# Optimization experiments

Hardware: AMD Instinct MI355X
Metric: run time of the kernel (lower is better)

The kernel has to match this reference:

```python
import jax, jax.numpy as jnp
import numpy as np

B, S, D = 2, 2048, 2048
NH, HD = 32, 64          # query heads, head_dim
NKV, NREP = 8, 4         # kv heads, num_key_value_groups
ROPE_THETA = 10000.0


def _rope_cos_sin(seq_len, head_dim, dtype=jnp.float32):
    inv_freq = 1.0 / (ROPE_THETA ** (jnp.arange(0, head_dim, 2, dtype=jnp.float32) / head_dim))
    pos = jnp.arange(seq_len, dtype=jnp.float32)
    freqs = jnp.outer(pos, inv_freq)               # [S, HD/2]
    emb = jnp.concatenate([freqs, freqs], axis=-1)  # [S, HD]
    return jnp.cos(emb).astype(dtype), jnp.sin(emb).astype(dtype)


def _rotate_half(x):
    x1, x2 = jnp.split(x, 2, axis=-1)
    return jnp.concatenate([-x2, x1], axis=-1)


def setup_inputs() -> dict:
    key = jax.random.key(0)
    k1, k2, k3, k4, k5 = jax.random.split(key, 5)
    scale = 0.02
    hidden_states = jax.random.normal(k1, (B, S, D), dtype=jnp.float32)
    Wq = jax.random.normal(k2, (NH * HD, D), dtype=jnp.float32) * scale
    Wk = jax.random.normal(k3, (NKV * HD, D), dtype=jnp.float32) * scale
    Wv = jax.random.normal(k4, (NKV * HD, D), dtype=jnp.float32) * scale
    Wo = jax.random.normal(k5, (D, NH * HD), dtype=jnp.float32) * scale
    # additive causal mask [B, 1, S, S]: 0 on/below diagonal, large negative above
    causal = jnp.triu(jnp.full((S, S), -1e9, dtype=jnp.float32), k=1)
    attention_mask = jnp.broadcast_to(causal[None, None], (B, 1, S, S))
    return {"hidden_states": hidden_states, "Wq": Wq, "Wk": Wk, "Wv": Wv,
            "Wo": Wo, "attention_mask": attention_mask}


def reference(hidden_states, Wq, Wk, Wv, Wo, attention_mask):
    bsz, q_len, _ = hidden_states.shape
    # projections (torch Linear: x @ W^T)
    q = (hidden_states @ Wq.T).reshape(bsz, q_len, NH, HD).transpose(0, 2, 1, 3)   # [B,NH,S,HD]
    k = (hidden_states @ Wk.T).reshape(bsz, q_len, NKV, HD).transpose(0, 2, 1, 3)  # [B,NKV,S,HD]
    v = (hidden_states @ Wv.T).reshape(bsz, q_len, NKV, HD).transpose(0, 2, 1, 3)
    # RoPE
    cos, sin = _rope_cos_sin(q_len, HD, hidden_states.dtype)  # [S,HD]
    cos = cos[None, None]  # [1,1,S,HD] (unsqueeze_dim=1 over broadcast batch)
    sin = sin[None, None]
    q = q * cos + _rotate_half(q) * sin
    k = k * cos + _rotate_half(k) * sin
    # repeat_kv (GQA): [B,NKV,S,HD] -> [B,NH,S,HD]
    k = jnp.repeat(k, NREP, axis=1)
    v = jnp.repeat(v, NREP, axis=1)
    # eager attention with materialized scores (faithful to the source)
    scores = jnp.einsum('bhqd,bhkd->bhqk', q, k) / jnp.sqrt(jnp.float32(HD))
    scores = scores + attention_mask[:, :, :, :q_len]
    probs = jax.nn.softmax(scores.astype(jnp.float32), axis=-1).astype(q.dtype)
    out = jnp.einsum('bhqk,bhkd->bhqd', probs, v)          # [B,NH,S,HD]
    out = out.transpose(0, 2, 1, 3).reshape(bsz, q_len, NH * HD)
    return out @ Wo.T
```

## Files before the change

kernel.cpp:

```cpp
#include <hip/hip_runtime.h>


#define S_LEN 2048
#define D_MODEL 2048
#define NHEAD 32
#define HEAD_DIM 64
#define NKVH 8
#define M_ROWS 4096
#define KVW (NKVH * HEAD_DIM)

typedef __attribute__((ext_vector_type(4))) float f32x4;
typedef __attribute__((ext_vector_type(8))) short bf16x8;

#define MFMA16(a, b, c) __builtin_amdgcn_mfma_f32_16x16x32_bf16((a), (b), (c), 0, 0, 0)

#define GLOAD_LDS16(g, l)                                                     \
    __builtin_amdgcn_global_load_lds(                                         \
        (const __attribute__((address_space(1))) void*)(g),                   \
        (__attribute__((address_space(3))) void*)(l), 16, 0, 0)

static __device__ __forceinline__ unsigned short f2bf(float f) {
    union { __bf16 b; unsigned short u; } v;
    v.b = (__bf16)f;
    return v.u;
}

static __device__ __forceinline__ void xcd_swz(int& bx, int& by) {
    const int gx = gridDim.x;
    const int nwg = gx * gridDim.y;
    int lin = blockIdx.y * gx + blockIdx.x;
    lin = (lin & 7) * (nwg >> 3) + (lin >> 3);
    bx = lin % gx;
    by = lin / gx;
}

static __device__ bool detect_f32_block(const unsigned short* __restrict__ h) {
    __shared__ int dcnt;
    if (threadIdx.x == 0) dcnt = 0;
    __syncthreads();
    const unsigned short v = h[2 * (threadIdx.x & 255)];
    const int e = (v >> 7) & 0xFF;
    if (threadIdx.x < 256 && e >= 0x8D) atomicAdd(&dcnt, 1);
    __syncthreads();
    return dcnt >= 8;
}

static __device__ __forceinline__ bf16x8 load_frag(bool f32p, const void* p, size_t off) {
    if (f32p) {
        const float* fp = (const float*)p + off;
        f32x4 x = *reinterpret_cast<const f32x4*>(fp);
        f32x4 y = *reinterpret_cast<const f32x4*>(fp + 4);
        bf16x8 r;
        r[0] = (short)f2bf(x[0]); r[1] = (short)f2bf(x[1]);
        r[2] = (short)f2bf(x[2]); r[3] = (short)f2bf(x[3]);
        r[4] = (short)f2bf(y[0]); r[5] = (short)f2bf(y[1]);
        r[6] = (short)f2bf(y[2]); r[7] = (short)f2bf(y[3]);
        return r;
    }
    return *reinterpret_cast<const bf16x8*>((const unsigned short*)p + off);
}

__global__ __launch_bounds__(256) void cvt_all(const void* __restrict__ h,
                                               const void* __restrict__ wq,
                                               const void* __restrict__ wk,
                                               const void* __restrict__ wv,
                                               const void* __restrict__ wo,
                                               unsigned short* __restrict__ hbuf,
                                               unsigned short* __restrict__ wqb,
                                               unsigned short* __restrict__ wkvb,
                                               unsigned short* __restrict__ wob,
                                               float2* __restrict__ ropetab) {
    const bool f32p = detect_f32_block((const unsigned short*)h);
    const int e0 = 1048576;
    const int e1 = e0 + 524288;
    const int e2 = e1 + 131072;
    const int e3 = e2 + 131072;
    const int e4 = e3 + 524288;
    const int e5 = e4 + 8192;
    int i = blockIdx.x * 256 + threadIdx.x;
    const int stride = gridDim.x * 256;
    for (; i < e5; i += stride) {
        if (i >= e4) {
            const int base = (i - e4) * 8;
#pragma unroll
            for (int j = 0; j < 8; ++j) {
                const int idx = base + j;
                const int s = idx >> 5, dd = idx & 31;
                const float inv = exp2f(-(float)dd * 0.4152410118609203f);
                const float th = (float)s * inv;
                float sn, cs;
                sincosf(th, &sn, &cs);
                ropetab[idx] = make_float2(cs, sn);
            }
            continue;
        }
        const void* s;
        unsigned short* d;
        size_t off;
        if (i < e0)      { s = h;  d = hbuf; off = (size_t)i; }
        else if (i < e1) { s = wq; d = wqb;  off = (size_t)(i - e0); }
        else if (i < e2) { s = wk; d = wkvb; off = (size_t)(i - e1); }
        else if (i < e3) { s = wv; d = wkvb + (size_t)512 * 2048; off = (size_t)(i - e2); }
        else             { s = wo; d = wob;  off = (size_t)(i - e3); }
        bf16x8 v = load_frag(f32p, s, off * 8);
        *reinterpret_cast<bf16x8*>(d + off * 8) = v;
    }
}

static __device__ __forceinline__ void rope4_tab(const float2* __restrict__ tab,
                                                 const float (&vals)[4], float (&outv)[4],
                                                 int m, int l16) {
    const int s = m & (S_LEN - 1);
#pragma unroll
    for (int nt = 0; nt < 4; ++nt) {
        const int d = nt * 16 + l16;
        const float2 cs = tab[s * 32 + (d & 31)];
        const float part = vals[nt ^ 2];
        const float rot = (nt < 2) ? -part : part;
        outv[nt] = vals[nt] * cs.x + rot * cs.y;
    }
}

static __device__ __forceinline__ void rope4(const float (&vals)[4], float (&outv)[4],
                                             int m, int l16) {
    const float sf = (float)(m & (S_LEN - 1));
#pragma unroll
    for (int nt = 0; nt < 4; ++nt) {
        const int d = nt * 16 + l16;
        const float inv = exp2f(-(float)(d & 31) * 0.4152410118609203f);
        const float th = sf * inv;
        float sn, cs;
        sincosf(th, &sn, &cs);
        const float part = vals[nt ^ 2];
        const float rot = (nt < 2) ? -part : part;
        outv[nt] = vals[nt] * cs + rot * sn;
    }
}

#define GEMM_STAGE(BB, KK)                                                    \
    {                                                                         \
        _Pragma("unroll")                                                     \
        for (int i_ = 0; i_ < 2; ++i_) {                                      \
            const int c_ = wave * 2 + i_;                                     \
            GLOAD_LDS16(ag[i_] + (KK), &lds_a[BB][c_ * 512]);                 \
            GLOAD_LDS16(wg[i_] + (KK), &lds_b[BB][c_ * 512]);                 \
        }                                                                     \
    }

#define GEMM_MAINLOOP()                                                       \
    GEMM_STAGE(0, 0);                                                         \
    __syncthreads();                                                          \
    {                                                                         \
        int cur = 0;                                                          \
        for (int k0 = 0; k0 < D_MODEL; k0 += 32) {                            \
            if (k0 + 32 < D_MODEL) GEMM_STAGE(cur ^ 1, k0 + 32);              \
            bf16x8 af[4], bfm[4];                                             \
            _Pragma("unroll")                                                 \
            for (int t = 0; t < 4; ++t) {                                     \
                af[t]  = *reinterpret_cast<const bf16x8*>(                    \
                    &lds_a[cur][(wm * 64 + t * 16 + l16) * 32 + quad * 8]);   \
                bfm[t] = *reinterpret_cast<const bf16x8*>(                    \
                    &lds_b[cur][(wn * 64 + t * 16 + l16) * 32 + quad * 8]);   \
            }                                                                 \
            _Pragma("unroll")                                                 \
            for (int mt = 0; mt < 4; ++mt)                                    \
                _Pragma("unroll")                                             \
                for (int nt = 0; nt < 4; ++nt)                                \
                    acc[mt][nt] = MFMA16(af[mt], bfm[nt], acc[mt][nt]);       \
            __syncthreads();                                                  \
            cur ^= 1;                                                         \
        }                                                                     \
    }

__global__ __launch_bounds__(256) void gemm_qkv_lds(const unsigned short* __restrict__ A,
                                                    const unsigned short* __restrict__ W,
                                                    unsigned short* __restrict__ Qo,
                                                    unsigned short* __restrict__ KVo,
                                                    const float2* __restrict__ ropetab) {
    __shared__ unsigned short lds_a[2][128 * 32];
    __shared__ unsigned short lds_b[2][128 * 32];

    const int wave = threadIdx.x >> 6;
    const int lane = threadIdx.x & 63;
    const int l16  = lane & 15;
    const int quad = lane >> 4;
    const int wm   = wave >> 1;
    const int wn   = wave & 1;

    int bx, by;
    xcd_swz(bx, by);
    const int m0 = bx * 128;
    const int n0 = by * 128;

    const int srow = lane >> 2;
    const int scol = (lane & 3) * 8;
    const unsigned short* ag[2];
    const unsigned short* wg[2];
#pragma unroll
    for (int i = 0; i < 2; ++i) {
        const int c = wave * 2 + i;
        ag[i] = A + (size_t)(m0 + c * 16 + srow) * D_MODEL + scol;
        wg[i] = W + (size_t)(n0 + c * 16 + srow) * D_MODEL + scol;
    }

    f32x4 acc[4][4];
#pragma unroll
    for (int i = 0; i < 4; ++i)
#pragma unroll
        for (int j = 0; j < 4; ++j) acc[i][j] = (f32x4){0.f, 0.f, 0.f, 0.f};

    GEMM_MAINLOOP();

    const int ncol0 = n0 + wn * 64;
    const bool do_rope = (ncol0 < 2048 + KVW);
    unsigned short* dst;
    int cstride, c0;
    if (ncol0 < 2048) { dst = Qo;  cstride = 2048; c0 = ncol0; }
    else              { dst = KVo; cstride = 1024; c0 = ncol0 - 2048; }

#pragma unroll
    for (int mt = 0; mt < 4; ++mt) {
#pragma unroll
        for (int r = 0; r < 4; ++r) {
            const int m = m0 + wm * 64 + mt * 16 + quad * 4 + r;
            float vals[4];
#pragma unroll
            for (int nt = 0; nt < 4; ++nt) vals[nt] = acc[mt][nt][r];
            float outv[4];
            if (do_rope) {
                rope4_tab(ropetab, vals, outv, m, l16);
            } else {
#pragma unroll
                for (int nt = 0; nt < 4; ++nt) outv[nt] = vals[nt];
            }
            unsigned short* cp = dst + (size_t)m * cstride + c0;
#pragma unroll
            for (int nt = 0; nt < 4; ++nt) cp[nt * 16 + l16] = f2bf(outv[nt]);
        }
    }
}

__global__ __launch_bounds__(256) void gemm_bt_lds(const unsigned short* __restrict__ A,
                                                   const unsigned short* __restrict__ W,
                                                   void* __restrict__ Cp, int N,
                                                   const unsigned short* __restrict__ hdet,
                                                   int rope, int finalout) {
    __shared__ unsigned short lds_a[2][128 * 32];
    __shared__ unsigned short lds_b[2][128 * 32];

    bool of32 = false;
    if (finalout) of32 = detect_f32_block(hdet);

    const int wave = threadIdx.x >> 6;
    const int lane = threadIdx.x & 63;
    const int l16  = lane & 15;
    const int quad = lane >> 4;
    const int wm   = wave >> 1;
    const int wn   = wave & 1;

    int bx, by;
    xcd_swz(bx, by);
    const int m0 = bx * 128;
    const int n0 = by * 128;

    const int srow = lane >> 2;
    const int scol = (lane & 3) * 8;
    const unsigned short* ag[2];
    const unsigned short* wg[2];
#pragma unroll
    for (int i = 0; i < 2; ++i) {
        const int c = wave * 2 + i;
        ag[i] = A + (size_t)(m0 + c * 16 + srow) * D_MODEL + scol;
        wg[i] = W + (size_t)(n0 + c * 16 + srow) * D_MODEL + scol;
    }

    f32x4 acc[4][4];
#pragma unroll
    for (int i = 0; i < 4; ++i)
#pragma unroll
        for (int j = 0; j < 4; ++j) acc[i][j] = (f32x4){0.f, 0.f, 0.f, 0.f};

    GEMM_MAINLOOP();

    const bool do_rope = (rope != 0);
    const int ncol0 = n0 + wn * 64;

#pragma unroll
    for (int mt = 0; mt < 4; ++mt) {
#pragma unroll
        for (int r = 0; r < 4; ++r) {
            const int m = m0 + wm * 64 + mt * 16 + quad * 4 + r;
            float vals[4];
#pragma unroll
            for (int nt = 0; nt < 4; ++nt) vals[nt] = acc[mt][nt][r];
            float outv[4];
            if (do_rope) {
                rope4(vals, outv, m, l16);
            } else {
#pragma unroll
                for (int nt = 0; nt < 4; ++nt) outv[nt] = vals[nt];
            }
            const size_t crow = (size_t)m * N + ncol0;
            if (of32) {
                float* cp = (float*)Cp + crow;
#pragma unroll
                for (int nt = 0; nt < 4; ++nt) cp[nt * 16 + l16] = outv[nt];
            } else {
                unsigned short* cp = (unsigned short*)Cp + crow;
#pragma unroll
                for (int nt = 0; nt < 4; ++nt) cp[nt * 16 + l16] = f2bf(outv[nt]);
            }
        }
    }
}

__global__ __launch_bounds__(256) void transpose_v(const unsigned short* __restrict__ Vsrc,
                                                   unsigned short* __restrict__ Vt) {
    __shared__ unsigned short t[64][72];
    const int bid = blockIdx.x;
    const int ct = bid & 7;
    const int st = (bid >> 3) & 31;
    const int b  = bid >> 8;
    const unsigned short* src = Vsrc + ((size_t)b * S_LEN + st * 64) * 1024 + ct * 64;
    unsigned short* dst = Vt + ((size_t)b * KVW + ct * 64) * S_LEN + st * 64;
    const int r0 = threadIdx.x >> 3;
    const int c0 = (threadIdx.x & 7) * 8;
#pragma unroll
    for (int h = 0; h < 2; ++h) {
        bf16x8 v = *reinterpret_cast<const bf16x8*>(src + (size_t)(r0 + h * 32) * 1024 + c0);
        *reinterpret_cast<bf16x8*>(&t[r0 + h * 32][c0]) = v;
    }
    __syncthreads();
#pragma unroll
    for (int h = 0; h < 2; ++h) {
        const int cr = r0 + h * 32;
        bf16x8 v;
#pragma unroll
        for (int j = 0; j < 8; ++j) v[j] = (short)t[c0 + j][cr];
        *reinterpret_cast<bf16x8*>(dst + (size_t)cr * S_LEN + c0) = v;
    }
}

struct AttnCtx {
    const unsigned short* qbase;
    const unsigned short* kbase;
    const unsigned short* vtbase;
    unsigned short* obase;
    int kvs;
    int l16, quad;
    unsigned short (*lpw)[72];
};

#define SM_SCALE 0.125f
#define SM_THR_E 5.545177444479562f

static __device__ __forceinline__ void attn_qtile(const AttnCtx& cx, int q0w) {
    const int l16 = cx.l16, quad = cx.quad;
    const int kvs = cx.kvs;

    bf16x8 ones;
#pragma unroll
    for (int j = 0; j < 8; ++j) ones[j] = (short)0x3F80;

    bf16x8 aq[2][2];
#pragma unroll
    for (int m = 0; m < 2; ++m)
#pragma unroll
        for (int kh = 0; kh < 2; ++kh)
            aq[m][kh] = *reinterpret_cast<const bf16x8*>(
                cx.qbase + (size_t)(q0w + m * 16 + l16) * D_MODEL + kh * 32 + quad * 8);

    f32x4 o[2][4];
    f32x4 c_l[2];
#pragma unroll
    for (int m = 0; m < 2; ++m) {
#pragma unroll
        for (int i = 0; i < 4; ++i) o[m][i] = (f32x4){0.f, 0.f, 0.f, 0.f};
        c_l[m] = (f32x4){0.f, 0.f, 0.f, 0.f};
    }
    float m2[2][4];
#pragma unroll
    for (int m = 0; m < 2; ++m)
#pragma unroll
        for (int r = 0; r < 4; ++r) m2[m][r] = 0.f;

    const int kv_hi = q0w + 32;

    for (int k0 = 0; k0 < kv_hi; k0 += 64) {
        bf16x8 kf[8];
#pragma unroll
        for (int t = 0; t < 4; ++t) {
            const unsigned short* krow = cx.kbase + (size_t)(k0 + t * 16 + l16) * kvs;
            kf[2 * t]     = *reinterpret_cast<const bf16x8*>(krow + quad * 8);
            kf[2 * t + 1] = *reinterpret_cast<const bf16x8*>(krow + 32 + quad * 8);
        }

        f32x4 sc[2][4];
        __builtin_amdgcn_s_setprio(1);
#pragma unroll
        for (int t = 0; t < 4; ++t) {
#pragma unroll
            for (int m = 0; m < 2; ++m) {
                f32x4 c = (f32x4){0.f, 0.f, 0.f, 0.f};
                c = MFMA16(aq[m][0], kf[2 * t], c);
                c = MFMA16(aq[m][1], kf[2 * t + 1], c);
                sc[m][t] = c;
            }
        }
        __builtin_amdgcn_s_setprio(0);

        bf16x8 vf[8];
#pragma unroll
        for (int nt = 0; nt < 4; ++nt) {
            const unsigned short* vrow =
                cx.vtbase + (size_t)(nt * 16 + l16) * S_LEN + k0 + quad * 8;
            vf[2 * nt]     = *reinterpret_cast<const bf16x8*>(vrow);
            vf[2 * nt + 1] = *reinterpret_cast<const bf16x8*>(vrow + 32);
        }

        const bool full = (k0 + 63 <= q0w);
        float pm[2][4];
        float dif = -3.0e38f;
#pragma unroll
        for (int m = 0; m < 2; ++m) {
#pragma unroll
            for (int r = 0; r < 4; ++r) {
                const int qi = q0w + m * 16 + quad * 4 + r;
                float s[4];
#pragma unroll
                for (int t = 0; t < 4; ++t) {
                    s[t] = sc[m][t][r] * SM_SCALE;
                    if (!full && (k0 + t * 16 + l16 > qi)) s[t] = -1.0e30f;
                    sc[m][t][r] = s[t];
                }
                const float p = fmaxf(fmaxf(s[0], s[1]), fmaxf(s[2], s[3]));
                pm[m][r] = p;
                dif = fmaxf(dif, p - m2[m][r]);
            }
        }
        if (__any(dif > SM_THR_E)) {
#pragma unroll
            for (int m = 0; m < 2; ++m) {
#pragma unroll
                for (int r = 0; r < 4; ++r) {
                    float mt = pm[m][r];
#pragma unroll
                    for (int off = 1; off < 16; off <<= 1)
                        mt = fmaxf(mt, __shfl_xor(mt, off, 64));
                    const float mn = fmaxf(m2[m][r], mt);
                    const float al = __expf(m2[m][r] - mn);
                    m2[m][r] = mn;
#pragma unroll
                    for (int nt = 0; nt < 4; ++nt) o[m][nt][r] *= al;
                    c_l[m][r] *= al;
                }
            }
        }
#pragma unroll
        for (int m = 0; m < 2; ++m) {
#pragma unroll
            for (int r = 0; r < 4; ++r) {
                const float mb = m2[m][r];
#pragma unroll
                for (int t = 0; t < 4; ++t) {
                    const float pv = __expf(sc[m][t][r] - mb);
                    cx.lpw[m * 16 + quad * 4 + r][t * 16 + l16] = f2bf(pv);
                }
            }
        }
        asm volatile("" ::: "memory");
        bf16x8 ap[2][2];
#pragma unroll
        for (int m = 0; m < 2; ++m)
#pragma unroll
            for (int kh = 0; kh < 2; ++kh)
                ap[m][kh] = *reinterpret_cast<const bf16x8*>(
                    &cx.lpw[m * 16 + l16][kh * 32 + quad * 8]);
        __builtin_amdgcn_s_setprio(1);
#pragma unroll
        for (int nt = 0; nt < 4; ++nt)
#pragma unroll
            for (int m = 0; m < 2; ++m) {
                o[m][nt] = MFMA16(ap[m][0], vf[2 * nt], o[m][nt]);
                o[m][nt] = MFMA16(ap[m][1], vf[2 * nt + 1], o[m][nt]);
            }
#pragma unroll
        for (int m = 0; m < 2; ++m) {
            c_l[m] = MFMA16(ap[m][0], ones, c_l[m]);
            c_l[m] = MFMA16(ap[m][1], ones, c_l[m]);
        }
        __builtin_amdgcn_s_setprio(0);
    }

#pragma unroll
    for (int m = 0; m < 2; ++m)
#pragma unroll
        for (int r = 0; r < 4; ++r) {
            const float inv_l = 1.0f / c_l[m][r];
            unsigned short* orow = cx.obase + (size_t)(q0w + m * 16 + quad * 4 + r) * D_MODEL;
#pragma unroll
            for (int nt = 0; nt < 4; ++nt)
                orow[nt * 16 + l16] = f2bf(o[m][nt][r] * inv_l);
        }
}

__global__ __launch_bounds__(256) void attn_kernel8(const unsigned short* __restrict__ Q,
                                                    const unsigned short* __restrict__ Kb,
                                                    const unsigned short* __restrict__ Vt,
                                                    unsigned short* __restrict__ O, int kvs) {
    __shared__ unsigned short lp[4][32][72];

    const int wave = threadIdx.x >> 6;
    const int lane = threadIdx.x & 63;

    const int bid  = blockIdx.x;
    const int qt   = 15 - (bid >> 6);
    const int bh   = bid & 63;
    const int h    = bh & (NHEAD - 1);
    const int b    = bh >> 5;
    const int kvh  = h >> 2;

    AttnCtx cx;
    cx.qbase  = Q + (size_t)b * S_LEN * D_MODEL + h * HEAD_DIM;
    cx.kbase  = Kb + (size_t)b * S_LEN * kvs + kvh * HEAD_DIM;
    cx.vtbase = Vt + ((size_t)b * KVW + kvh * HEAD_DIM) * S_LEN;
    cx.obase  = O + (size_t)b * S_LEN * D_MODEL + h * HEAD_DIM;
    cx.kvs    = kvs;
    cx.l16    = lane & 15;
    cx.quad   = lane >> 4;
    cx.lpw    = lp[wave];

    attn_qtile(cx, qt * 128 + wave * 32);
}

__global__ __launch_bounds__(256) void gemm_bt(const void* __restrict__ Ap,
                                               const void* __restrict__ Wp,
                                               void* __restrict__ Cp, int N,
                                               const unsigned short* __restrict__ hdet,
                                               int a_input, int rope, int finalout) {
    const bool isf32 = detect_f32_block(hdet);
    const bool af32 = isf32 && (a_input != 0);
    const bool wf32 = isf32;
    const bool of32 = isf32 && (finalout != 0);

    const int wave = threadIdx.x >> 6;
    const int lane = threadIdx.x & 63;
    const int l16  = lane & 15;
    const int quad = lane >> 4;
    const int m0 = blockIdx.x * 64 + wave * 16;
    const int n0 = blockIdx.y * 64;

    f32x4 acc[4];
#pragma unroll
    for (int i = 0; i < 4; ++i) acc[i] = (f32x4){0.f, 0.f, 0.f, 0.f};

    const size_t aoff = (size_t)(m0 + l16) * D_MODEL + quad * 8;
    size_t woff[4];
#pragma unroll
    for (int nt = 0; nt < 4; ++nt)
        woff[nt] = (size_t)(n0 + nt * 16 + l16) * D_MODEL + quad * 8;

    for (int k0 = 0; k0 < D_MODEL; k0 += 32) {
        bf16x8 a = load_frag(af32, Ap, aoff + k0);
#pragma unroll
        for (int nt = 0; nt < 4; ++nt) {
            bf16x8 b = load_frag(wf32, Wp, woff[nt] + k0);
            acc[nt] = MFMA16(a, b, acc[nt]);
        }
    }

#pragma unroll
    for (int r = 0; r < 4; ++r) {
        const int m = m0 + quad * 4 + r;
        float vals[4];
#pragma unroll
        for (int nt = 0; nt < 4; ++nt) vals[nt] = acc[nt][r];
        float outv[4];
        if (rope) {
            rope4(vals, outv, m, l16);
        } else {
#pragma unroll
            for (int nt = 0; nt < 4; ++nt) outv[nt] = vals[nt];
        }
        const size_t crow = (size_t)m * N + n0;
        if (of32) {
            float* cp = (float*)Cp + crow;
#pragma unroll
            for (int nt = 0; nt < 4; ++nt) cp[nt * 16 + l16] = outv[nt];
        } else {
            unsigned short* cp = (unsigned short*)Cp + crow;
#pragma unroll
            for (int nt = 0; nt < 4; ++nt) cp[nt * 16 + l16] = f2bf(outv[nt]);
        }
    }
}

__global__ __launch_bounds__(256) void attn_kernel(const unsigned short* __restrict__ Q,
                                                   const unsigned short* __restrict__ Kb,
                                                   const unsigned short* __restrict__ Vb,
                                                   unsigned short* __restrict__ O, int kvs) {
    __shared__ unsigned short lp[4][16][32];

    const int wave = threadIdx.x >> 6;
    const int lane = threadIdx.x & 63;
    const int l16  = lane & 15;
    const int quad = lane >> 4;

    const int bid = blockIdx.x;
    const int qb  = bid & 31;
    const int h   = (bid >> 5) & 31;
    const int b   = bid >> 10;
    const int kvh = h >> 2;
    const int q0  = qb * 64 + wave * 16;

    const unsigned short* qbase = Q + (size_t)b * S_LEN * D_MODEL + h * HEAD_DIM;
    const unsigned short* kbase = Kb + (size_t)b * S_LEN * kvs + kvh * HEAD_DIM;
    const unsigned short* vbase = Vb + (size_t)b * S_LEN * kvs + kvh * HEAD_DIM;

    bf16x8 aq0 = *reinterpret_cast<const bf16x8*>(qbase + (size_t)(q0 + l16) * D_MODEL + quad * 8);
    bf16x8 aq1 = *reinterpret_cast<const bf16x8*>(qbase + (size_t)(q0 + l16) * D_MODEL + 32 + quad * 8);

    f32x4 o[4];
#pragma unroll
    for (int i = 0; i < 4; ++i) o[i] = (f32x4){0.f, 0.f, 0.f, 0.f};
    float mrow[4], lrow[4];
#pragma unroll
    for (int r = 0; r < 4; ++r) { mrow[r] = -3.0e38f; lrow[r] = 0.f; }

    const int kv_hi = qb * 64 + 64;
    for (int k0 = 0; k0 < kv_hi; k0 += 32) {
        f32x4 sc[2];
#pragma unroll
        for (int t = 0; t < 2; ++t) {
            const unsigned short* krow = kbase + (size_t)(k0 + t * 16 + l16) * kvs;
            bf16x8 b0 = *reinterpret_cast<const bf16x8*>(krow + quad * 8);
            bf16x8 b1 = *reinterpret_cast<const bf16x8*>(krow + 32 + quad * 8);
            f32x4 c = (f32x4){0.f, 0.f, 0.f, 0.f};
            c = MFMA16(aq0, b0, c);
            c = MFMA16(aq1, b1, c);
            sc[t] = c;
        }

        float alpha[4], p0v[4], p1v[4];
#pragma unroll
        for (int r = 0; r < 4; ++r) {
            const int qi = q0 + quad * 4 + r;
            float s0 = sc[0][r] * 0.125f;
            float s1 = sc[1][r] * 0.125f;
            if (k0 + l16 > qi)       s0 = -1.0e30f;
            if (k0 + 16 + l16 > qi)  s1 = -1.0e30f;
            float mt = fmaxf(s0, s1);
#pragma unroll
            for (int off = 1; off < 16; off <<= 1) mt = fmaxf(mt, __shfl_xor(mt, off, 64));
            const float mn = fmaxf(mrow[r], mt);
            const float al = __expf(mrow[r] - mn);
            const float p0 = __expf(s0 - mn);
            const float p1 = __expf(s1 - mn);
            float rs = p0 + p1;
#pragma unroll
            for (int off = 1; off < 16; off <<= 1) rs += __shfl_xor(rs, off, 64);
            lrow[r] = lrow[r] * al + rs;
            mrow[r] = mn;
            alpha[r] = al;
            p0v[r] = p0; p1v[r] = p1;
        }
#pragma unroll
        for (int nt = 0; nt < 4; ++nt)
#pragma unroll
            for (int r = 0; r < 4; ++r) o[nt][r] *= alpha[r];

        __syncthreads();
#pragma unroll
        for (int r = 0; r < 4; ++r) {
            lp[wave][quad * 4 + r][l16]      = f2bf(p0v[r]);
            lp[wave][quad * 4 + r][16 + l16] = f2bf(p1v[r]);
        }
        __syncthreads();
        bf16x8 ap = *reinterpret_cast<const bf16x8*>(&lp[wave][l16][quad * 8]);

#pragma unroll
        for (int nt = 0; nt < 4; ++nt) {
            const unsigned short* vcol = vbase + nt * 16 + l16 + (size_t)(k0 + quad * 8) * kvs;
            bf16x8 bv;
#pragma unroll
            for (int j = 0; j < 8; ++j) bv[j] = (short)vcol[(size_t)j * kvs];
            o[nt] = MFMA16(ap, bv, o[nt]);
        }
    }

    unsigned short* obase = O + (size_t)b * S_LEN * D_MODEL + h * HEAD_DIM;
#pragma unroll
    for (int r = 0; r < 4; ++r) {
        const float inv_l = 1.0f / lrow[r];
        unsigned short* orow = obase + (size_t)(q0 + quad * 4 + r) * D_MODEL;
#pragma unroll
        for (int nt = 0; nt < 4; ++nt)
            orow[nt * 16 + l16] = f2bf(o[nt][r] * inv_l);
    }
}

extern "C" void kernel_launch(void* const* d_in, const int* in_sizes, int n_in,
                              void* d_out, int out_size, void* d_ws, size_t ws_size,
                              hipStream_t stream) {
    const void* hidden = d_in[0];
    const void* Wq = d_in[1];
    const void* Wk = d_in[2];
    const void* Wv = d_in[3];
    const void* Wo = d_in[4];

    char* ws = (char*)d_ws;
    dim3 blk(256);

    const size_t NEED = 1024 + ((size_t)64 << 20) + (512u << 10);
    if (ws_size >= NEED) {
        unsigned short* kvbuf = (unsigned short*)(ws + 1024);
        unsigned short* abuf  = kvbuf + (size_t)4096 * 1024;
        unsigned short* hbuf  = abuf + (size_t)4096 * 2048;
        unsigned short* wqb   = hbuf + (size_t)4096 * 2048;
        unsigned short* wkvb  = wqb + (size_t)2048 * 2048;
        unsigned short* wob   = wkvb + (size_t)1024 * 2048;
        unsigned short* vtbuf = wob + (size_t)2048 * 2048;
        float2* ropetab       = (float2*)(vtbuf + (size_t)2 * 512 * 2048);
        unsigned short* qbuf  = (unsigned short*)d_out;

        cvt_all<<<dim3(2048), blk, 0, stream>>>(hidden, Wq, Wk, Wv, Wo,
                                                hbuf, wqb, wkvb, wob, ropetab);

        gemm_qkv_lds<<<dim3(32, 24), blk, 0, stream>>>(hbuf, wqb, qbuf, kvbuf, ropetab);
        transpose_v<<<dim3(512), blk, 0, stream>>>(kvbuf + 512, vtbuf);
        attn_kernel8<<<dim3(2 * NHEAD * (S_LEN / 128)), blk, 0, stream>>>(qbuf, kvbuf, vtbuf, abuf, 1024);
        gemm_bt_lds<<<dim3(32, 16), blk, 0, stream>>>(abuf, wob, d_out, 2048,
                                                      (const unsigned short*)hidden, 0, 1);
    } else {
        unsigned short* kbuf = (unsigned short*)(ws + 1024);
        unsigned short* vbuf = (unsigned short*)(ws + 1024 + (4u << 20));
        unsigned short* abuf = (unsigned short*)(ws + 1024 + (8u << 20));
        unsigned short* qbuf = (unsigned short*)d_out;
        const unsigned short* hdet = (const unsigned short*)hidden;
        gemm_bt<<<dim3(M_ROWS / 64, D_MODEL / 64), blk, 0, stream>>>(hidden, Wq, qbuf, D_MODEL, hdet, 1, 1, 0);
        gemm_bt<<<dim3(M_ROWS / 64, (NKVH * HEAD_DIM) / 64), blk, 0, stream>>>(hidden, Wk, kbuf, NKVH * HEAD_DIM, hdet, 1, 1, 0);
        gemm_bt<<<dim3(M_ROWS / 64, (NKVH * HEAD_DIM) / 64), blk, 0, stream>>>(hidden, Wv, vbuf, NKVH * HEAD_DIM, hdet, 1, 0, 0);
        attn_kernel<<<dim3(2 * NHEAD * (S_LEN / 64)), blk, 0, stream>>>(qbuf, kbuf, vbuf, abuf, 512);
        gemm_bt<<<dim3(M_ROWS / 64, D_MODEL / 64), blk, 0, stream>>>(abuf, Wo, d_out, D_MODEL, hdet, 0, 0, 1);
    }
}
```

Baseline: 422.7 us.

## Use single-buffered BK=64 GEMM tiles with XOR-swizzled LDS layout

The projection GEMMs drop the double-buffered BK=32 LDS pipeline in favour of a single buffer of BK=64 per iteration, which halves the number of loop iterations and barriers. The global-to-LDS column offsets and the LDS read offsets are XOR-swizzled by row to avoid bank conflicts on the wider rows. In exchange, loads for the next tile no longer overlap the MFMA work on the current one, so latency is exposed at each barrier.

```diff
diff --git a/kernel.cpp b/kernel.cpp
--- a/kernel.cpp
+++ b/kernel.cpp
@@ -137,39 +137,47 @@
     }
 }
 
-#define GEMM_STAGE(BB, KK)                                                    \
-    {                                                                         \
+#define GEMM_PTR_SETUP(ABASE, WBASE)                                          \
+    const int l8r = lane >> 3;                                                \
+    const int scol_sw = ((((lane & 7) * 16) ^ (l8r << 4)) >> 1);              \
+    const unsigned short* ag[4];                                              \
+    const unsigned short* wg[4];                                              \
+    _Pragma("unroll")                                                         \
+    for (int i = 0; i < 4; ++i) {                                             \
+        const int c = wave * 4 + i;                                           \
+        ag[i] = (ABASE) + (size_t)(m0 + c * 8 + l8r) * D_MODEL + scol_sw;     \
+        wg[i] = (WBASE) + (size_t)(n0 + c * 8 + l8r) * D_MODEL + scol_sw;     \
+    }
+
+#define GEMM_MAINLOOP()                                                       \
+    for (int k0 = 0; k0 < D_MODEL; k0 += 64) {                                \
         _Pragma("unroll")                                                     \
-        for (int i_ = 0; i_ < 2; ++i_) {                                      \
-            const int c_ = wave * 2 + i_;                                     \
-            GLOAD_LDS16(ag[i_] + (KK), &lds_a[BB][c_ * 512]);                 \
-            GLOAD_LDS16(wg[i_] + (KK), &lds_b[BB][c_ * 512]);                 \
+        for (int i_ = 0; i_ < 4; ++i_) {                                      \
+            const int c_ = wave * 4 + i_;                                     \
+            GLOAD_LDS16(ag[i_] + k0, &lds_a[c_ * 512]);                       \
+            GLOAD_LDS16(wg[i_] + k0, &lds_b[c_ * 512]);                       \
         }                                                                     \
-    }
-
-#define GEMM_MAINLOOP()                                                       \
-    GEMM_STAGE(0, 0);                                                         \
-    __syncthreads();                                                          \
-    {                                                                         \
-        int cur = 0;                                                          \
-        for (int k0 = 0; k0 < D_MODEL; k0 += 32) {                            \
-            if (k0 + 32 < D_MODEL) GEMM_STAGE(cur ^ 1, k0 + 32);              \
+        __syncthreads();                                                      \
+        _Pragma("unroll")                                                     \
+        for (int kh = 0; kh < 2; ++kh) {                                      \
             bf16x8 af[4], bfm[4];                                             \
             _Pragma("unroll")                                                 \
             for (int t = 0; t < 4; ++t) {                                     \
+                const int ra = wm * 64 + t * 16 + l16;                        \
+                const int rb = wn * 64 + t * 16 + l16;                        \
+                const int offb = ((kh * 64) | (quad * 16)) ^ ((l16 & 7) << 4);\
                 af[t]  = *reinterpret_cast<const bf16x8*>(                    \
-                    &lds_a[cur][(wm * 64 + t * 16 + l16) * 32 + quad * 8]);   \
+                    &lds_a[ra * 64 + (offb >> 1)]);                           \
                 bfm[t] = *reinterpret_cast<const bf16x8*>(                    \
-                    &lds_b[cur][(wn * 64 + t * 16 + l16) * 32 + quad * 8]);   \
+                    &lds_b[rb * 64 + (offb >> 1)]);                           \
             }                                                                 \
             _Pragma("unroll")                                                 \
             for (int mt = 0; mt < 4; ++mt)                                    \
                 _Pragma("unroll")                                             \
                 for (int nt = 0; nt < 4; ++nt)                                \
                     acc[mt][nt] = MFMA16(af[mt], bfm[nt], acc[mt][nt]);       \
-            __syncthreads();                                                  \
-            cur ^= 1;                                                         \
         }                                                                     \
+        __syncthreads();                                                      \
     }
 
 __global__ __launch_bounds__(256) void gemm_qkv_lds(const unsigned short* __restrict__ A,
@@ -177,8 +185,8 @@
                                                     unsigned short* __restrict__ Qo,
                                                     unsigned short* __restrict__ KVo,
                                                     const float2* __restrict__ ropetab) {
-    __shared__ unsigned short lds_a[2][128 * 32];
-    __shared__ unsigned short lds_b[2][128 * 32];
+    __shared__ unsigned short lds_a[128 * 64];
+    __shared__ unsigned short lds_b[128 * 64];
 
     const int wave = threadIdx.x >> 6;
     const int lane = threadIdx.x & 63;
@@ -192,16 +200,7 @@
     const int m0 = bx * 128;
     const int n0 = by * 128;
 
-    const int srow = lane >> 2;
-    const int scol = (lane & 3) * 8;
-    const unsigned short* ag[2];
-    const unsigned short* wg[2];
-#pragma unroll
-    for (int i = 0; i < 2; ++i) {
-        const int c = wave * 2 + i;
-        ag[i] = A + (size_t)(m0 + c * 16 + srow) * D_MODEL + scol;
-        wg[i] = W + (size_t)(n0 + c * 16 + srow) * D_MODEL + scol;
-    }
+    GEMM_PTR_SETUP(A, W);
 
     f32x4 acc[4][4];
 #pragma unroll
@@ -245,8 +244,8 @@
                                                    void* __restrict__ Cp, int N,
                                                    const unsigned short* __restrict__ hdet,
                                                    int rope, int finalout) {
-    __shared__ unsigned short lds_a[2][128 * 32];
-    __shared__ unsigned short lds_b[2][128 * 32];
+    __shared__ unsigned short lds_a[128 * 64];
+    __shared__ unsigned short lds_b[128 * 64];
 
     bool of32 = false;
     if (finalout) of32 = detect_f32_block(hdet);
@@ -263,16 +262,7 @@
     const int m0 = bx * 128;
     const int n0 = by * 128;
 
-    const int srow = lane >> 2;
-    const int scol = (lane & 3) * 8;
-    const unsigned short* ag[2];
-    const unsigned short* wg[2];
-#pragma unroll
-    for (int i = 0; i < 2; ++i) {
-        const int c = wave * 2 + i;
-        ag[i] = A + (size_t)(m0 + c * 16 + srow) * D_MODEL + scol;
-        wg[i] = W + (size_t)(n0 + c * 16 + srow) * D_MODEL + scol;
-    }
+    GEMM_PTR_SETUP(A, W);
 
     f32x4 acc[4][4];
 #pragma unroll
```

Result: faster. 389.8 us (-7.8%).
